# Kernel optimization log

Hardware: AMD Instinct MI355X
Metric: run time of the kernel (lower is better)

## Reference

```python
import jax, jax.numpy as jnp
import numpy as np

K = 16  # neighbors per node (dgl.knn_graph k)


def _knn_indices(centers, k):
    # pairwise squared distances [N, N]
    sq = jnp.sum(centers * centers, axis=1)
    d2 = sq[:, None] + sq[None, :] - 2.0 * (centers @ centers.T)
    # k nearest (includes self at distance ~0), edges: neighbor(src) -> node(dst)
    _, idx = jax.lax.top_k(-d2, k)  # [N, k]
    return idx


def _graph_conv(h, idx, src_norm, dst_norm, W, b):
    # DGL GraphConv, norm='both': D_out^{-1/2} A D_in^{-1/2} H W + b
    hs = h * src_norm[:, None]          # scale by out-degree^{-1/2}
    agg = jnp.sum(hs[idx], axis=1)      # sum over k neighbors -> [N, F]
    agg = agg * dst_norm                # in-degree is exactly k for knn graph
    return agg @ W + b


def setup_inputs() -> dict:
    key = jax.random.key(0)
    ks = jax.random.split(key, 8)
    N, D, H = 20000, 128, 256
    s_in, s_h = 1.0 / np.sqrt(D), 1.0 / np.sqrt(H)
    return {
        "x": jax.random.normal(ks[0], (N, D), dtype=jnp.float32),
        "centers": jax.random.normal(ks[1], (N, 3), dtype=jnp.float32),
        "W0": jax.random.normal(ks[2], (D, H), dtype=jnp.float32) * s_in,
        "b0": jnp.zeros((H,), dtype=jnp.float32),
        "W1": jax.random.normal(ks[3], (H, H), dtype=jnp.float32) * s_h,
        "b1": jnp.zeros((H,), dtype=jnp.float32),
        "W2": jax.random.normal(ks[4], (H, H), dtype=jnp.float32) * s_h,
        "b2": jnp.zeros((H,), dtype=jnp.float32),
        "Wf": jax.random.normal(ks[5], (H, 1), dtype=jnp.float32) * s_h,
        "bf": jnp.zeros((1,), dtype=jnp.float32),
    }


def reference(x, centers, W0, b0, W1, b1, W2, b2, Wf, bf):
    N = x.shape[0]
    idx = _knn_indices(centers, K)  # [N, K] src nodes per dst node
    # out-degree of each node = number of times it appears as a neighbor
    out_deg = jnp.zeros((N,), dtype=x.dtype).at[idx.reshape(-1)].add(1.0)
    src_norm = jax.lax.rsqrt(jnp.maximum(out_deg, 1.0))
    dst_norm = 1.0 / jnp.sqrt(jnp.asarray(K, dtype=x.dtype))  # in-degree == K
    h = x
    for W, b in ((W0, b0), (W1, b1), (W2, b2)):
        h = jax.nn.relu(_graph_conv(h, idx, src_norm, dst_norm, W, b))
    logits = (h @ Wf + bf).squeeze(-1)  # [N]
    return jax.nn.sigmoid(logits)
```

## Files before the change

### kernel.cpp

```cpp
#include <hip/hip_runtime.h>
#include <math.h>

#define KNN 16
#define G 32
#define G3 32768
#define MRING 31
#define FLTMAX 3.402823466e+38f

typedef __attribute__((ext_vector_type(8))) short short8x;
typedef __attribute__((ext_vector_type(4))) float f32x4;

__device__ __forceinline__ unsigned short bf16rn(float x) {
  unsigned u = __float_as_uint(x);
  unsigned r = (u + 0x7FFFu + ((u >> 16) & 1u)) >> 16;
  return (unsigned short)r;
}
__device__ __forceinline__ float bf16tof(unsigned short h) {
  return __uint_as_float(((unsigned)h) << 16);
}

__device__ __forceinline__ unsigned fkey(float f) {
  unsigned u = __float_as_uint(f);
  return (u & 0x80000000u) ? ~u : (u | 0x80000000u);
}
__device__ __forceinline__ float funkey(unsigned u) {
  unsigned b = (u & 0x80000000u) ? (u & 0x7FFFFFFFu) : ~u;
  return __uint_as_float(b);
}

__device__ __forceinline__ void cell_of(float x, float y, float z, const float* P,
                                        int& cx, int& cy, int& cz) {
  cx = min(G - 1, max(0, (int)((x - P[0]) * P[3])));
  cy = min(G - 1, max(0, (int)((y - P[1]) * P[4])));
  cz = min(G - 1, max(0, (int)((z - P[2]) * P[5])));
}

__global__ void init_kernel(int* __restrict__ counts, int* __restrict__ cursor,
                            unsigned* __restrict__ bbox) {
  int t = blockIdx.x * blockDim.x + threadIdx.x;
  if (t < G3) counts[t] = 0;
  int u = t - G3;
  if (u >= 0 && u < G3) cursor[u] = 0;
  if (t == 0) {
    for (int k = 0; k < 3; ++k) { bbox[k] = 0xFFFFFFFFu; bbox[3 + k] = 0u; }
  }
}

__global__ void prep_kernel(const float* __restrict__ centers,
                            float4* __restrict__ cpack,
                            int* __restrict__ deg, unsigned* __restrict__ bbox, int n) {
  #pragma clang fp contract(off)
  int i = blockIdx.x * blockDim.x + threadIdx.x;
  if (i < n) {
    float x = centers[3 * i], y = centers[3 * i + 1], z = centers[3 * i + 2];
    float sq = (x * x + y * y) + z * z;
    cpack[i] = make_float4(x, y, z, sq);
    deg[i] = 0;
    atomicMin(&bbox[0], fkey(x));
    atomicMin(&bbox[1], fkey(y));
    atomicMin(&bbox[2], fkey(z));
    atomicMax(&bbox[3], fkey(x));
    atomicMax(&bbox[4], fkey(y));
    atomicMax(&bbox[5], fkey(z));
  }
}

__global__ void params_kernel(const unsigned* __restrict__ bbox, float* __restrict__ P) {
  if (threadIdx.x == 0 && blockIdx.x == 0) {
    float xmin = funkey(bbox[0]), ymin = funkey(bbox[1]), zmin = funkey(bbox[2]);
    float xmax = funkey(bbox[3]), ymax = funkey(bbox[4]), zmax = funkey(bbox[5]);
    float ex = fmaxf(xmax - xmin, 1e-9f);
    float ey = fmaxf(ymax - ymin, 1e-9f);
    float ez = fmaxf(zmax - zmin, 1e-9f);
    P[0] = xmin; P[1] = ymin; P[2] = zmin;
    P[3] = (float)G / ex; P[4] = (float)G / ey; P[5] = (float)G / ez;
    P[6] = ex / (float)G; P[7] = ey / (float)G; P[8] = ez / (float)G;
    P[9] = fminf(P[6], fminf(P[7], P[8]));
  }
}

__global__ void count_kernel(const float4* __restrict__ cpack, const float* __restrict__ P,
                             int* __restrict__ counts, int n) {
  int i = blockIdx.x * blockDim.x + threadIdx.x;
  if (i >= n) return;
  float4 c = cpack[i];
  int cx, cy, cz; cell_of(c.x, c.y, c.z, P, cx, cy, cz);
  atomicAdd(&counts[(cz * G + cy) * G + cx], 1);
}

__global__ __launch_bounds__(1024) void scan_kernel(const int* __restrict__ counts,
                                                    int* __restrict__ starts,
                                                    int2* __restrict__ cellinfo) {
  __shared__ int sh[1024];
  int t = threadIdx.x;
  int base = t * 32;
  int loc[32];
  int cnts[32];
  int s = 0;
  #pragma unroll
  for (int u = 0; u < 32; ++u) {
    cnts[u] = counts[base + u];
    loc[u] = s; s += cnts[u];
  }
  sh[t] = s;
  __syncthreads();
  for (int off = 1; off < 1024; off <<= 1) {
    int v = (t >= off) ? sh[t - off] : 0;
    __syncthreads();
    sh[t] += v;
    __syncthreads();
  }
  int pre = (t == 0) ? 0 : sh[t - 1];
  #pragma unroll
  for (int u = 0; u < 32; ++u) {
    int st = pre + loc[u];
    starts[base + u] = st;
    cellinfo[base + u] = make_int2(st, cnts[u]);
  }
}

__global__ void scatter_kernel(const float4* __restrict__ cpack, const float* __restrict__ P,
                               const int* __restrict__ starts, int* __restrict__ cursor,
                               int* __restrict__ sid, int* __restrict__ inv,
                               float4* __restrict__ spack, int n) {
  int i = blockIdx.x * blockDim.x + threadIdx.x;
  if (i >= n) return;
  float4 c = cpack[i];
  int cx, cy, cz; cell_of(c.x, c.y, c.z, P, cx, cy, cz);
  int cell = (cz * G + cy) * G + cx;
  int slot = starts[cell] + atomicAdd(&cursor[cell], 1);
  sid[slot] = i;
  inv[i] = slot;
  spack[slot] = c;
}

__global__ __launch_bounds__(64) void query_kernel(
    const float4* __restrict__ spack, const int* __restrict__ sid,
    const int* __restrict__ inv, const int2* __restrict__ cellinfo,
    const float* __restrict__ P, int* __restrict__ knn_idx,
    int* __restrict__ deg, int n) {
  #pragma clang fp contract(off)
  __shared__ unsigned long long lsk[KNN][64];
  const int lane = threadIdx.x;
  const int g = blockIdx.x;
  if (g >= n) return;
  const float4 q = spack[g];
  const float xmin = P[0], ymin = P[1], zmin = P[2];
  const float wx = P[6], wy = P[7], wz = P[8], wmin = P[9];
  int cx, cy, cz; cell_of(q.x, q.y, q.z, P, cx, cy, cz);

  int cnt = 0;
  unsigned long long wkey = 0; int wslot = 0;
  unsigned long long minkey = ~0ull; int minslot = 0;

  for (int m = 1; m <= MRING; ++m) {
    if (m >= 2) {
      float b = (float)(m - 1) * wmin;
      float b2 = b * b * 0.999f;
      unsigned long long tk = ((unsigned long long)fkey(b2)) << 32;
      int c = 0;
      for (int t = 0; t < cnt; ++t) c += (lsk[t][lane] < tk) ? 1 : 0;
      #pragma unroll
      for (int off = 1; off < 64; off <<= 1) c += __shfl_xor(c, off);
      if (c >= KNN) break;
    }
    float lw = (cnt == KNN) ? funkey((unsigned)(wkey >> 32)) : FLTMAX;
    #pragma unroll
    for (int off = 1; off < 64; off <<= 1) lw = fminf(lw, __shfl_xor(lw, off));

    const int ncells = (m == 1) ? 27 : (24 * m * m + 2);
    for (int cb = 0; cb < ncells; cb += 64) {
      int f = cb + lane;
      int ccnt = 0, cs0 = 0;
      if (f < ncells) {
        int dx, dy, dz;
        if (m == 1) {
          dz = f / 9 - 1; int rem = f % 9; dy = rem / 3 - 1; dx = rem % 3 - 1;
        } else {
          int side = 2 * m + 1;
          int S1 = side * side;
          if (f < 2 * S1) {
            dz = (f < S1) ? -m : m;
            int i2 = (f < S1) ? f : f - S1;
            dy = i2 / side - m; dx = i2 % side - m;
          } else {
            int r = f - 2 * S1;
            int layer = r / (8 * m);
            int t2 = r - layer * 8 * m;
            dz = layer - (m - 1);
            if (t2 < side) { dy = -m; dx = t2 - m; }
            else if (t2 < 2 * side) { dy = m; dx = (t2 - side) - m; }
            else { int u = t2 - 2 * side; dx = (u & 1) ? m : -m; dy = (u >> 1) - (m - 1); }
          }
        }
        int x = cx + dx, y = cy + dy, z = cz + dz;
        if (x >= 0 && x < G && y >= 0 && y < G && z >= 0 && z < G) {
          int cell = (z * G + y) * G + x;
          int2 ci = cellinfo[cell];
          if (ci.y > 0) {
            float lox = xmin + (float)x * wx;
            float loy = ymin + (float)y * wy;
            float loz = zmin + (float)z * wz;
            float ddx = fmaxf(fmaxf(lox - q.x, q.x - (lox + wx)), 0.f);
            float ddy = fmaxf(fmaxf(loy - q.y, q.y - (loy + wy)), 0.f);
            float ddz = fmaxf(fmaxf(loz - q.z, q.z - (loz + wz)), 0.f);
            float cd2 = ddx * ddx + ddy * ddy + ddz * ddz;
            if (!(cd2 * 0.999f > lw)) { ccnt = ci.y; cs0 = ci.x; }
          }
        }
      }
      int inc = ccnt;
      #pragma unroll
      for (int off = 1; off < 64; off <<= 1) {
        int t = __shfl_up(inc, off);
        if (lane >= off) inc += t;
      }
      int total = __shfl(inc, 63);
      if (total == 0) continue;
      unsigned seg = ((unsigned)(inc - ccnt) << 16) | (unsigned)cs0;
      const int tmax = total - 1;

      int fc = lane;
      int fcc = min(fc, tmax);
      int lo = 0;
      #pragma unroll
      for (int s = 32; s >= 1; s >>= 1) {
        int cand = lo + s;
        unsigned o = __shfl(seg, cand & 63);
        if (cand < 64 && (int)(o >> 16) <= fcc) lo = cand;
      }
      unsigned o2 = __shfl(seg, lo);
      int src = (int)(o2 & 0xFFFFu) + (fcc - (int)(o2 >> 16));
      float4 c4 = spack[src];
      int j = sid[src];
      const int nloop = (total + 63) >> 6;
      for (int it = 0; it < nloop; ++it) {
        int fn = fc + 64;
        int fnc = min(fn, tmax);
        int lo2 = 0;
        #pragma unroll
        for (int s = 32; s >= 1; s >>= 1) {
          int cand = lo2 + s;
          unsigned o = __shfl(seg, cand & 63);
          if (cand < 64 && (int)(o >> 16) <= fnc) lo2 = cand;
        }
        unsigned o3 = __shfl(seg, lo2);
        int srcn = (int)(o3 & 0xFFFFu) + (fnc - (int)(o3 >> 16));
        float4 c4n = spack[srcn];
        int jn = sid[srcn];
        if (fc < total) {
          float dot = fmaf(q.z, c4.z, fmaf(q.y, c4.y, q.x * c4.x));
          float d2 = (q.w + c4.w) - 2.0f * dot;
          unsigned long long key =
              (((unsigned long long)fkey(d2)) << 32) | (unsigned)j;
          if (cnt < KNN) {
            lsk[cnt][lane] = key;
            if (key < minkey) { minkey = key; minslot = cnt; }
            ++cnt;
            if (cnt == KNN) {
              wkey = 0; wslot = 0;
              #pragma unroll
              for (int u = 0; u < KNN; ++u) {
                unsigned long long k2 = lsk[u][lane];
                if (k2 > wkey) { wkey = k2; wslot = u; }
              }
            }
          } else if (key < wkey) {
            lsk[wslot][lane] = key;
            if (key < minkey) { minkey = key; minslot = wslot; }
            wkey = 0;
            #pragma unroll
            for (int u = 0; u < KNN; ++u) {
              unsigned long long k2 = lsk[u][lane];
              if (k2 > wkey) { wkey = k2; wslot = u; }
            }
          }
        }
        fc = fn; c4 = c4n; j = jn;
      }
    }
  }

  unsigned long long mykey = 0;
  for (int t = 0; t < KNN; ++t) {
    unsigned long long k = minkey; int src = lane;
    #pragma unroll
    for (int off = 1; off < 64; off <<= 1) {
      unsigned long long ok = __shfl_xor(k, off);
      int os = __shfl_xor(src, off);
      if (ok < k) { k = ok; src = os; }
    }
    if (lane == t) mykey = k;
    if (lane == src) {
      lsk[minslot][lane] = ~0ull;
      minkey = ~0ull; minslot = 0;
      for (int u = 0; u < cnt; ++u) {
        unsigned long long kk = lsk[u][lane];
        if (kk < minkey) { minkey = kk; minslot = u; }
      }
    }
  }
  if (lane < KNN) {
    int j = (int)(unsigned)(mykey & 0xFFFFFFFFull);
    int js = inv[j];
    knn_idx[g * KNN + lane] = js;
    atomicAdd(&deg[js], 1);
  }
}

__global__ void norm_kernel(const int* __restrict__ deg, float* __restrict__ srcn, int n) {
  int i = blockIdx.x * blockDim.x + threadIdx.x;
  if (i < n) {
    float d = (float)max(deg[i], 1);
    srcn[i] = 1.0f / sqrtf(d);
  }
}

__global__ void split_w_kernel(const float* __restrict__ W,
                               unsigned short* __restrict__ wbh,
                               unsigned short* __restrict__ wbl, int K) {
  int t = blockIdx.x * blockDim.x + threadIdx.x;
  int noct = (K >> 5) * 1024;
  if (t >= noct) return;
  int kblk = t >> 10;
  int g = (t >> 6) & 15;
  int l = t & 63;
  int n = ((g >> 2) << 6) + ((g & 3) << 4) + (l & 15);
  int kbase = (kblk << 5) + ((l >> 4) << 3);
  #pragma unroll
  for (int j = 0; j < 8; ++j) {
    float w = W[(kbase + j) * 256 + n];
    unsigned short hi = bf16rn(w);
    wbh[t * 8 + j] = hi;
    wbl[t * 8 + j] = bf16rn(w - bf16tof(hi));
  }
}

__device__ __forceinline__ int xcd_swizzle(int b, int grid8) {
  int nch = grid8 >> 3;
  return (b & 7) * nch + (b >> 3);
}

template <int F>
__global__ __launch_bounds__(256) void agg_kernel(const float* __restrict__ h,
                                                  const int* __restrict__ rmap,
                                                  const float* __restrict__ srcn,
                                                  const int* __restrict__ idx,
                                                  unsigned short* __restrict__ ah,
                                                  unsigned short* __restrict__ al,
                                                  int n) {
  const int lane = threadIdx.x & 63;
  const int wv = threadIdx.x >> 6;
  const int eb = xcd_swizzle(blockIdx.x, gridDim.x);
  const int i = eb * 4 + wv;
  if (i >= n) return;
  constexpr int V = F / 64;
  if constexpr (V == 4) {
    float4 acc = make_float4(0.f, 0.f, 0.f, 0.f);
    #pragma unroll
    for (int k = 0; k < KNN; ++k) {
      int s = idx[i * KNN + k];
      float sn = srcn[s];
      int row = rmap ? rmap[s] : s;
      float4 hv = ((const float4*)(h + (size_t)row * F))[lane];
      acc.x = fmaf(sn, hv.x, acc.x);
      acc.y = fmaf(sn, hv.y, acc.y);
      acc.z = fmaf(sn, hv.z, acc.z);
      acc.w = fmaf(sn, hv.w, acc.w);
    }
    acc.x *= 0.25f; acc.y *= 0.25f; acc.z *= 0.25f; acc.w *= 0.25f;
    ushort4 hh, ll;
    hh.x = bf16rn(acc.x); ll.x = bf16rn(acc.x - bf16tof(hh.x));
    hh.y = bf16rn(acc.y); ll.y = bf16rn(acc.y - bf16tof(hh.y));
    hh.z = bf16rn(acc.z); ll.z = bf16rn(acc.z - bf16tof(hh.z));
    hh.w = bf16rn(acc.w); ll.w = bf16rn(acc.w - bf16tof(hh.w));
    ((ushort4*)(ah + (size_t)i * F))[lane] = hh;
    ((ushort4*)(al + (size_t)i * F))[lane] = ll;
  } else {
    float2 acc = make_float2(0.f, 0.f);
    #pragma unroll
    for (int k = 0; k < KNN; ++k) {
      int s = idx[i * KNN + k];
      float sn = srcn[s];
      int row = rmap ? rmap[s] : s;
      float2 hv = ((const float2*)(h + (size_t)row * F))[lane];
      acc.x = fmaf(sn, hv.x, acc.x);
      acc.y = fmaf(sn, hv.y, acc.y);
    }
    acc.x *= 0.25f; acc.y *= 0.25f;
    ushort2 hh, ll;
    hh.x = bf16rn(acc.x); ll.x = bf16rn(acc.x - bf16tof(hh.x));
    hh.y = bf16rn(acc.y); ll.y = bf16rn(acc.y - bf16tof(hh.y));
    ((ushort2*)(ah + (size_t)i * F))[lane] = hh;
    ((ushort2*)(al + (size_t)i * F))[lane] = ll;
  }
}

__global__ __launch_bounds__(256) void gemm_mfma(
    const unsigned short* __restrict__ ah, const unsigned short* __restrict__ al,
    const unsigned short* __restrict__ wbh, const unsigned short* __restrict__ wbl,
    const float* __restrict__ bias, float* __restrict__ C, int M, int Kd) {
  __shared__ unsigned short sa_h[2][64][8];
  __shared__ unsigned short sa_l[2][64][8];
  __shared__ unsigned short sb_h[16][64][8];
  __shared__ unsigned short sb_l[16][64][8];
  const int tid = threadIdx.x;
  const int lane = tid & 63;
  const int w = tid >> 6;
  const int eb = xcd_swizzle(blockIdx.x, gridDim.x);
  const int mt0 = eb * 32;
  if (mt0 >= M) return;

  f32x4 acc[2][4];
  #pragma unroll
  for (int ms = 0; ms < 2; ++ms)
    #pragma unroll
    for (int ns = 0; ns < 4; ++ns) acc[ms][ns] = (f32x4){0.f, 0.f, 0.f, 0.f};

  const int nkb = Kd >> 5;
  for (int kit = 0; kit < nkb; ++kit) {
    const int k0 = kit << 5;
    if (tid < 128) {
      int msub = tid >> 6, l = tid & 63;
      int row = mt0 + (msub << 4) + (l & 15);
      int kk = k0 + ((l >> 4) << 3);
      if (row < M) {
        *(uint4*)&sa_h[msub][l][0] = *(const uint4*)(ah + (size_t)row * Kd + kk);
        *(uint4*)&sa_l[msub][l][0] = *(const uint4*)(al + (size_t)row * Kd + kk);
      } else {
        uint4 z = make_uint4(0, 0, 0, 0);
        *(uint4*)&sa_h[msub][l][0] = z;
        *(uint4*)&sa_l[msub][l][0] = z;
      }
    }
    #pragma unroll
    for (int o = tid; o < 1024; o += 256) {
      size_t off = ((size_t)kit * 1024 + o) * 8;
      *(uint4*)&sb_h[o >> 6][o & 63][0] = *(const uint4*)(wbh + off);
      *(uint4*)&sb_l[o >> 6][o & 63][0] = *(const uint4*)(wbl + off);
    }
    __syncthreads();
    short8x a_h0 = *(const short8x*)&sa_h[0][lane][0];
    short8x a_h1 = *(const short8x*)&sa_h[1][lane][0];
    short8x a_l0 = *(const short8x*)&sa_l[0][lane][0];
    short8x a_l1 = *(const short8x*)&sa_l[1][lane][0];
    #pragma unroll
    for (int ns = 0; ns < 4; ++ns) {
      short8x b_h = *(const short8x*)&sb_h[w * 4 + ns][lane][0];
      short8x b_l = *(const short8x*)&sb_l[w * 4 + ns][lane][0];
      acc[0][ns] = __builtin_amdgcn_mfma_f32_16x16x32_bf16(a_h0, b_h, acc[0][ns], 0, 0, 0);
      acc[0][ns] = __builtin_amdgcn_mfma_f32_16x16x32_bf16(a_h0, b_l, acc[0][ns], 0, 0, 0);
      acc[0][ns] = __builtin_amdgcn_mfma_f32_16x16x32_bf16(a_l0, b_h, acc[0][ns], 0, 0, 0);
      acc[1][ns] = __builtin_amdgcn_mfma_f32_16x16x32_bf16(a_h1, b_h, acc[1][ns], 0, 0, 0);
      acc[1][ns] = __builtin_amdgcn_mfma_f32_16x16x32_bf16(a_h1, b_l, acc[1][ns], 0, 0, 0);
      acc[1][ns] = __builtin_amdgcn_mfma_f32_16x16x32_bf16(a_l1, b_h, acc[1][ns], 0, 0, 0);
    }
    __syncthreads();
  }

  const int col = lane & 15;
  const int rq = lane >> 4;
  #pragma unroll
  for (int ms = 0; ms < 2; ++ms) {
    #pragma unroll
    for (int ns = 0; ns < 4; ++ns) {
      int nn = (w << 6) + (ns << 4) + col;
      float bi = bias[nn];
      #pragma unroll
      for (int r = 0; r < 4; ++r) {
        int row = mt0 + (ms << 4) + (rq << 2) + r;
        if (row < M) C[(size_t)row * 256 + nn] = fmaxf(acc[ms][ns][r] + bi, 0.f);
      }
    }
  }
}

__global__ __launch_bounds__(256) void final_kernel(const float* __restrict__ h,
                                                    const int* __restrict__ sid,
                                                    const float* __restrict__ Wf,
                                                    const float* __restrict__ bf,
                                                    float* __restrict__ out, int n) {
  const int lane = threadIdx.x & 63;
  const int wv = threadIdx.x >> 6;
  const int eb = xcd_swizzle(blockIdx.x, gridDim.x);
  const int i = eb * 4 + wv;
  if (i >= n) return;
  float4 hv = *(const float4*)(h + (size_t)i * 256 + lane * 4);
  float4 wf = *(const float4*)(Wf + lane * 4);
  float p = hv.x * wf.x + hv.y * wf.y + hv.z * wf.z + hv.w * wf.w;
  #pragma unroll
  for (int off = 32; off > 0; off >>= 1) p += __shfl_down(p, off);
  if (lane == 0) out[sid[i]] = 1.0f / (1.0f + expf(-(p + bf[0])));
}

extern "C" void kernel_launch(void* const* d_in, const int* in_sizes, int n_in,
                              void* d_out, int out_size, void* d_ws, size_t ws_size,
                              hipStream_t stream) {
  const float* x = (const float*)d_in[0];
  const float* centers = (const float*)d_in[1];
  const float* W0 = (const float*)d_in[2];
  const float* b0 = (const float*)d_in[3];
  const float* W1 = (const float*)d_in[4];
  const float* b1 = (const float*)d_in[5];
  const float* W2 = (const float*)d_in[6];
  const float* b2 = (const float*)d_in[7];
  const float* Wf = (const float*)d_in[8];
  const float* bf = (const float*)d_in[9];
  float* out = (float*)d_out;

  const int N = in_sizes[1] / 3;

  char* p = (char*)d_ws;
  auto alloc = [&](size_t bytes) {
    void* r = (void*)p;
    p += (bytes + 255) & ~(size_t)255;
    return r;
  };
  float4* cpack = (float4*)alloc((size_t)N * 16);
  int* deg = (int*)alloc((size_t)N * 4);
  float* srcn = (float*)alloc((size_t)N * 4);
  int* idx = (int*)alloc((size_t)N * KNN * 4);
  unsigned short* ahb = (unsigned short*)alloc((size_t)N * 256 * 2);
  unsigned short* alb = (unsigned short*)alloc((size_t)N * 256 * 2);
  float* hA = (float*)alloc((size_t)N * 256 * 4);
  unsigned* bbox = (unsigned*)alloc(6 * 4);
  float* P = (float*)alloc(16 * 4);
  int* counts = (int*)alloc((size_t)G3 * 4);
  int* starts = (int*)alloc((size_t)G3 * 4);
  int* cursor = (int*)alloc((size_t)G3 * 4);
  int2* cellinfo = (int2*)alloc((size_t)G3 * 8);
  int* sid = (int*)alloc((size_t)N * 4);
  int* inv = (int*)alloc((size_t)N * 4);
  float4* spack = (float4*)alloc((size_t)N * 16);
  unsigned short* w0h = (unsigned short*)alloc(128 * 256 * 2);
  unsigned short* w0l = (unsigned short*)alloc(128 * 256 * 2);
  unsigned short* w1h = (unsigned short*)alloc(256 * 256 * 2);
  unsigned short* w1l = (unsigned short*)alloc(256 * 256 * 2);
  unsigned short* w2h = (unsigned short*)alloc(256 * 256 * 2);
  unsigned short* w2l = (unsigned short*)alloc(256 * 256 * 2);
  (void)ws_size; (void)n_in; (void)out_size;

  const int nb = (N + 255) / 256;

  init_kernel<<<256, 256, 0, stream>>>(counts, cursor, bbox);
  prep_kernel<<<nb, 256, 0, stream>>>(centers, cpack, deg, bbox, N);
  split_w_kernel<<<(128 / 32) * 1024 / 256, 256, 0, stream>>>(W0, w0h, w0l, 128);
  split_w_kernel<<<(256 / 32) * 1024 / 256, 256, 0, stream>>>(W1, w1h, w1l, 256);
  split_w_kernel<<<(256 / 32) * 1024 / 256, 256, 0, stream>>>(W2, w2h, w2l, 256);
  params_kernel<<<1, 64, 0, stream>>>(bbox, P);
  count_kernel<<<nb, 256, 0, stream>>>(cpack, P, counts, N);
  scan_kernel<<<1, 1024, 0, stream>>>(counts, starts, cellinfo);
  scatter_kernel<<<nb, 256, 0, stream>>>(cpack, P, starts, cursor, sid, inv, spack, N);
  query_kernel<<<N, 64, 0, stream>>>(spack, sid, inv, cellinfo, P, idx, deg, N);
  norm_kernel<<<nb, 256, 0, stream>>>(deg, srcn, N);

  const int agrid = ((N + 3) / 4 + 7) & ~7;
  const int ggrid = (((N + 31) / 32) + 7) & ~7;

  agg_kernel<128><<<agrid, 256, 0, stream>>>(x, sid, srcn, idx, ahb, alb, N);
  gemm_mfma<<<ggrid, 256, 0, stream>>>(ahb, alb, w0h, w0l, b0, hA, N, 128);

  agg_kernel<256><<<agrid, 256, 0, stream>>>(hA, nullptr, srcn, idx, ahb, alb, N);
  gemm_mfma<<<ggrid, 256, 0, stream>>>(ahb, alb, w1h, w1l, b1, hA, N, 256);

  agg_kernel<256><<<agrid, 256, 0, stream>>>(hA, nullptr, srcn, idx, ahb, alb, N);
  gemm_mfma<<<ggrid, 256, 0, stream>>>(ahb, alb, w2h, w2l, b2, hA, N, 256);

  final_kernel<<<agrid, 256, 0, stream>>>(hA, sid, Wf, bf, out, N);
}
```

Measured before the change: 478.2 us.

## Pack point id into spack, prefetch two ahead, two queries per block

Stores the original point index in the w component of the sorted point pack, so the query loop no longer makes a separate sid gather, and recomputes squared norms on the fly. The candidate loads are now prefetched two iterations ahead instead of one, and each 128-thread block handles two queries with one wave each, halving the block count. This aims to cut gather traffic and latency in the kNN query, at the cost of a few extra FLOPs per candidate and more registers.

```diff
diff --git a/kernel.cpp b/kernel.cpp
--- a/kernel.cpp
+++ b/kernel.cpp
@@ -33,6 +33,18 @@
   cx = min(G - 1, max(0, (int)((x - P[0]) * P[3])));
   cy = min(G - 1, max(0, (int)((y - P[1]) * P[4])));
   cz = min(G - 1, max(0, (int)((z - P[2]) * P[5])));
+}
+
+__device__ __forceinline__ int seg_lookup(unsigned seg, int f) {
+  int lo = 0;
+  #pragma unroll
+  for (int s = 32; s >= 1; s >>= 1) {
+    int cand = lo + s;
+    unsigned o = __shfl(seg, cand & 63);
+    if (cand < 64 && (int)(o >> 16) <= f) lo = cand;
+  }
+  unsigned o2 = __shfl(seg, lo);
+  return (int)(o2 & 0xFFFFu) + (f - (int)(o2 >> 16));
 }
 
 __global__ void init_kernel(int* __restrict__ counts, int* __restrict__ cursor,
@@ -131,20 +143,21 @@
   int slot = starts[cell] + atomicAdd(&cursor[cell], 1);
   sid[slot] = i;
   inv[i] = slot;
-  spack[slot] = c;
-}
-
-__global__ __launch_bounds__(64) void query_kernel(
-    const float4* __restrict__ spack, const int* __restrict__ sid,
-    const int* __restrict__ inv, const int2* __restrict__ cellinfo,
-    const float* __restrict__ P, int* __restrict__ knn_idx,
-    int* __restrict__ deg, int n) {
+  spack[slot] = make_float4(c.x, c.y, c.z, __int_as_float(i));
+}
+
+__global__ __launch_bounds__(128) void query_kernel(
+    const float4* __restrict__ spack, const int* __restrict__ inv,
+    const int2* __restrict__ cellinfo, const float* __restrict__ P,
+    int* __restrict__ knn_idx, int* __restrict__ deg, int n) {
   #pragma clang fp contract(off)
-  __shared__ unsigned long long lsk[KNN][64];
-  const int lane = threadIdx.x;
-  const int g = blockIdx.x;
+  __shared__ unsigned long long lsk[2][KNN][64];
+  const int lane = threadIdx.x & 63;
+  const int wv = threadIdx.x >> 6;
+  const int g = blockIdx.x * 2 + wv;
   if (g >= n) return;
   const float4 q = spack[g];
+  const float qsq = (q.x * q.x + q.y * q.y) + q.z * q.z;
   const float xmin = P[0], ymin = P[1], zmin = P[2];
   const float wx = P[6], wy = P[7], wz = P[8], wmin = P[9];
   int cx, cy, cz; cell_of(q.x, q.y, q.z, P, cx, cy, cz);
@@ -159,7 +172,7 @@
       float b2 = b * b * 0.999f;
       unsigned long long tk = ((unsigned long long)fkey(b2)) << 32;
       int c = 0;
-      for (int t = 0; t < cnt; ++t) c += (lsk[t][lane] < tk) ? 1 : 0;
+      for (int t = 0; t < cnt; ++t) c += (lsk[wv][t][lane] < tk) ? 1 : 0;
       #pragma unroll
       for (int off = 1; off < 64; off <<= 1) c += __shfl_xor(c, off);
       if (c >= KNN) break;
@@ -220,63 +233,46 @@
       unsigned seg = ((unsigned)(inc - ccnt) << 16) | (unsigned)cs0;
       const int tmax = total - 1;
 
-      int fc = lane;
-      int fcc = min(fc, tmax);
-      int lo = 0;
-      #pragma unroll
-      for (int s = 32; s >= 1; s >>= 1) {
-        int cand = lo + s;
-        unsigned o = __shfl(seg, cand & 63);
-        if (cand < 64 && (int)(o >> 16) <= fcc) lo = cand;
-      }
-      unsigned o2 = __shfl(seg, lo);
-      int src = (int)(o2 & 0xFFFFu) + (fcc - (int)(o2 >> 16));
-      float4 c4 = spack[src];
-      int j = sid[src];
+      int fc0 = lane;
+      float4 c40 = spack[seg_lookup(seg, min(fc0, tmax))];
+      int fc1 = lane + 64;
+      float4 c41 = spack[seg_lookup(seg, min(fc1, tmax))];
       const int nloop = (total + 63) >> 6;
       for (int it = 0; it < nloop; ++it) {
-        int fn = fc + 64;
-        int fnc = min(fn, tmax);
-        int lo2 = 0;
-        #pragma unroll
-        for (int s = 32; s >= 1; s >>= 1) {
-          int cand = lo2 + s;
-          unsigned o = __shfl(seg, cand & 63);
-          if (cand < 64 && (int)(o >> 16) <= fnc) lo2 = cand;
-        }
-        unsigned o3 = __shfl(seg, lo2);
-        int srcn = (int)(o3 & 0xFFFFu) + (fnc - (int)(o3 >> 16));
-        float4 c4n = spack[srcn];
-        int jn = sid[srcn];
-        if (fc < total) {
-          float dot = fmaf(q.z, c4.z, fmaf(q.y, c4.y, q.x * c4.x));
-          float d2 = (q.w + c4.w) - 2.0f * dot;
+        int fc2 = fc0 + 128;
+        float4 c42 = spack[seg_lookup(seg, min(fc2, tmax))];
+        if (fc0 < total) {
+          float dot = fmaf(q.z, c40.z, fmaf(q.y, c40.y, q.x * c40.x));
+          float csq = (c40.x * c40.x + c40.y * c40.y) + c40.z * c40.z;
+          float d2 = (qsq + csq) - 2.0f * dot;
+          int j = __float_as_int(c40.w);
           unsigned long long key =
               (((unsigned long long)fkey(d2)) << 32) | (unsigned)j;
           if (cnt < KNN) {
-            lsk[cnt][lane] = key;
+            lsk[wv][cnt][lane] = key;
             if (key < minkey) { minkey = key; minslot = cnt; }
             ++cnt;
             if (cnt == KNN) {
               wkey = 0; wslot = 0;
               #pragma unroll
               for (int u = 0; u < KNN; ++u) {
-                unsigned long long k2 = lsk[u][lane];
+                unsigned long long k2 = lsk[wv][u][lane];
                 if (k2 > wkey) { wkey = k2; wslot = u; }
               }
             }
           } else if (key < wkey) {
-            lsk[wslot][lane] = key;
+            lsk[wv][wslot][lane] = key;
             if (key < minkey) { minkey = key; minslot = wslot; }
             wkey = 0;
             #pragma unroll
             for (int u = 0; u < KNN; ++u) {
-              unsigned long long k2 = lsk[u][lane];
+              unsigned long long k2 = lsk[wv][u][lane];
               if (k2 > wkey) { wkey = k2; wslot = u; }
             }
           }
         }
-        fc = fn; c4 = c4n; j = jn;
+        fc0 = fc1; c40 = c41;
+        fc1 = fc2; c41 = c42;
       }
     }
   }
@@ -292,10 +288,10 @@
     }
     if (lane == t) mykey = k;
     if (lane == src) {
-      lsk[minslot][lane] = ~0ull;
+      lsk[wv][minslot][lane] = ~0ull;
       minkey = ~0ull; minslot = 0;
       for (int u = 0; u < cnt; ++u) {
-        unsigned long long kk = lsk[u][lane];
+        unsigned long long kk = lsk[wv][u][lane];
         if (kk < minkey) { minkey = kk; minslot = u; }
       }
     }
@@ -551,7 +547,7 @@
   count_kernel<<<nb, 256, 0, stream>>>(cpack, P, counts, N);
   scan_kernel<<<1, 1024, 0, stream>>>(counts, starts, cellinfo);
   scatter_kernel<<<nb, 256, 0, stream>>>(cpack, P, starts, cursor, sid, inv, spack, N);
-  query_kernel<<<N, 64, 0, stream>>>(spack, sid, inv, cellinfo, P, idx, deg, N);
+  query_kernel<<<(N + 1) / 2, 128, 0, stream>>>(spack, inv, cellinfo, P, idx, deg, N);
   norm_kernel<<<nb, 256, 0, stream>>>(deg, srcn, N);
 
   const int agrid = ((N + 3) / 4 + 7) & ~7;
```

Result: no change. 485.2 us (+1.5%).
